# Performance work log

Hardware: AMD Instinct MI355X
Metric: run time of the kernel (lower is better)

Reference implementation:

```python
import jax, jax.numpy as jnp
import numpy as np

B, L, D_MODEL, N_HEADS = 2, 2048, 1024, 16
RANK = max(N_HEADS, int(D_MODEL * 0.25))            # 256
RANK_PER_HEAD = RANK // N_HEADS                      # 16
HEAD_DIM = D_MODEL // N_HEADS                        # 64


def _rope_cos_sin(L, head_dim, dtype=jnp.float32):
    half = head_dim // 2
    theta = 1.0 / (10000.0 ** (jnp.arange(half, dtype=dtype) / half))
    angles = jnp.arange(L, dtype=dtype)[:, None] * theta[None, :]   # [L, half]
    return jnp.cos(angles), jnp.sin(angles)


def _apply_rope(x, cos, sin):
    # x: [B, L, H, D]; pairs (even, odd) rotated by per-position angle.
    B, L, H, D = x.shape
    xp = x.reshape(B, L, H, D // 2, 2)
    x0, x1 = xp[..., 0], xp[..., 1]
    c = cos[None, :, None, :]
    s = sin[None, :, None, :]
    r0 = x0 * c - x1 * s
    r1 = x0 * s + x1 * c
    return jnp.stack([r0, r1], axis=-1).reshape(B, L, H, D)


def setup_inputs() -> dict:
    key = jax.random.key(0)
    ks = jax.random.split(key, 7)
    x = jax.random.normal(ks[0], (B, L, D_MODEL), dtype=jnp.float32)
    mask = jax.random.randint(ks[1], (B, L), 0, 2, dtype=jnp.int32)
    scale = 0.02
    Wq = jax.random.normal(ks[2], (RANK, D_MODEL), dtype=jnp.float32) * scale
    Wk = jax.random.normal(ks[3], (RANK, D_MODEL), dtype=jnp.float32) * scale
    Wv = jax.random.normal(ks[4], (RANK, D_MODEL), dtype=jnp.float32) * scale
    xav_u = float(np.sqrt(6.0 / (HEAD_DIM + RANK_PER_HEAD)))
    U = jax.random.uniform(ks[5], (N_HEADS, HEAD_DIM, RANK_PER_HEAD), dtype=jnp.float32, minval=-xav_u, maxval=xav_u)
    V = jax.random.uniform(ks[6], (N_HEADS, RANK_PER_HEAD, HEAD_DIM), dtype=jnp.float32, minval=-xav_u, maxval=xav_u)
    return {"x": x, "Wq": Wq, "Wk": Wk, "Wv": Wv, "U": U, "V": V, "mask": mask}


def reference(x, Wq, Wk, Wv, U, V, mask):
    Bq, Lq, _ = x.shape
    H, HD, RH = U.shape
    q_low = (x @ Wq.T).reshape(Bq, Lq, H, RH)
    k_low = (x @ Wk.T).reshape(Bq, Lq, H, RH)
    v_low = (x @ Wv.T).reshape(Bq, Lq, H, RH)
    # up-project q/k to head_dim via shared U
    q = jnp.einsum('hdr,blhr->blhd', U, q_low)
    k = jnp.einsum('hdr,blhr->blhd', U, k_low)
    cos, sin = _rope_cos_sin(Lq, HD, x.dtype)
    q = _apply_rope(q, cos, sin)
    k = _apply_rope(k, cos, sin)
    attn = jnp.einsum('blhd,bmhd->bhlm', q, k) / jnp.sqrt(jnp.asarray(HD, x.dtype))
    key_mask = mask.astype(bool)[:, None, None, :]           # [B,1,1,M]
    attn = jnp.where(key_mask, attn, jnp.asarray(-jnp.inf, attn.dtype))
    attn = jax.nn.softmax(attn, axis=-1)
    out = jnp.einsum('bhlm,bmhr->blhr', attn, v_low)
    out = jnp.einsum('blhr,hrd->blhd', out, V)
    return out.reshape(Bq, Lq, H * HD)
```

## Files before the change

kernel.cpp:

```cpp
#include <hip/hip_runtime.h>
#include <hip/hip_bf16.h>

typedef unsigned short u16;
typedef unsigned int u32;
typedef __bf16 bf16x8 __attribute__((ext_vector_type(8)));
typedef float f32x4 __attribute__((ext_vector_type(4)));

#define NB 2
#define NL 2048
#define NDM 1024
#define NH 16
#define NHD 64
#define NRH 16
#define NCOL 2304

#define QSCL 0.18033688011112042f

#define AS1(p) ((const __attribute__((address_space(1))) void*)(p))
#define AS3(p) ((__attribute__((address_space(3))) void*)(p))

__device__ __forceinline__ u16 f2bf(float f) {
  u32 u = __builtin_bit_cast(u32, f);
  u32 r = (u + 0x7fffu + ((u >> 16) & 1u)) >> 16;
  return (u16)r;
}
__device__ __forceinline__ float bf2f(u16 b) {
  return __builtin_bit_cast(float, (u32)b << 16);
}

__global__ void k_prep_weff(const float* __restrict__ Wq, const float* __restrict__ Wk,
                            const float* __restrict__ Wv, const float* __restrict__ U,
                            u16* __restrict__ Wall) {
  int idx = blockIdx.x * 256 + threadIdx.x;
  int col = idx & 1023;
  int row = idx >> 10;
  float acc;
  if (row < 2048) {
    const float* W = (row < 1024) ? Wq : Wk;
    int rr = row & 1023;
    int h = rr >> 6, d = rr & 63;
    const float* Uh = U + (h * NHD + d) * NRH;
    const float* Wr = W + (size_t)(h * NRH) * NDM + col;
    acc = 0.f;
#pragma unroll
    for (int r = 0; r < 16; ++r) acc += Uh[r] * Wr[(size_t)r * NDM];
  } else {
    acc = Wv[(size_t)(row - 2048) * NDM + col];
  }
  Wall[idx] = f2bf(acc);
}

__global__ void k_cast_x(const float* __restrict__ x, u16* __restrict__ xb) {
  int i = blockIdx.x * 256 + threadIdx.x;
  float2 v = *(const float2*)(x + (size_t)i * 2);
  ushort2 o;
  o.x = f2bf(v.x);
  o.y = f2bf(v.y);
  *(ushort2*)(xb + (size_t)i * 2) = o;
}

__global__ void k_rope_tab(float* __restrict__ ctab, float* __restrict__ stab) {
  int i = blockIdx.x * 256 + threadIdx.x;
  if (i >= NL * 32) return;
  int l = i >> 5, j = i & 31;
  float theta = 1.0f / powf(10000.0f, (float)j * (1.0f / 32.0f));
  float ang = (float)l * theta;
  ctab[i] = cosf(ang);
  stab[i] = sinf(ang);
}

__global__ void k_fbias(const int* __restrict__ mask, float* __restrict__ fb) {
  int i = blockIdx.x * 256 + threadIdx.x;
  fb[i] = mask[i] ? 0.f : -1e30f;
}

__global__ __launch_bounds__(256) void k_gemm(const u16* __restrict__ A,
                                              const u16* __restrict__ Bm,
                                              u16* __restrict__ C) {
  __shared__ char lds[32768];
  const int tid = threadIdx.x;
  const int wave = tid >> 6, lane = tid & 63;
  const int bm = blockIdx.x, bn = blockIdx.y;
  const int wr = wave >> 1, wc = wave & 1;
  const char* Ag = (const char*)(A + (size_t)bm * 128 * NDM);
  const char* Bg = (const char*)(Bm + (size_t)bn * 128 * NDM);
  f32x4 acc[4][4] = {};
  for (int kt = 0; kt < 16; ++kt) {
    __syncthreads();
#pragma unroll
    for (int i = 0; i < 4; ++i) {
      int off = wave * 4096 + i * 1024 + lane * 16;
      int src = off ^ ((off >> 3) & 0x70);
      int ga = (src >> 7) * 2048 + kt * 128 + (src & 127);
      __builtin_amdgcn_global_load_lds(AS1(Ag + ga), AS3(lds + wave * 4096 + i * 1024), 16, 0, 0);
      __builtin_amdgcn_global_load_lds(AS1(Bg + ga), AS3(lds + 16384 + wave * 4096 + i * 1024), 16, 0, 0);
    }
    __syncthreads();
#pragma unroll
    for (int kk = 0; kk < 2; ++kk) {
      bf16x8 af[4], bfr[4];
#pragma unroll
      for (int m = 0; m < 4; ++m) {
        int row = wr * 64 + m * 16 + (lane & 15);
        int byte = row * 128 + kk * 64 + ((lane >> 4) << 4);
        af[m] = *(const bf16x8*)(lds + (byte ^ ((row & 7) << 4)));
      }
#pragma unroll
      for (int n = 0; n < 4; ++n) {
        int row = wc * 64 + n * 16 + (lane & 15);
        int byte = row * 128 + kk * 64 + ((lane >> 4) << 4);
        bfr[n] = *(const bf16x8*)(lds + 16384 + (byte ^ ((row & 7) << 4)));
      }
#pragma unroll
      for (int m = 0; m < 4; ++m)
#pragma unroll
        for (int n = 0; n < 4; ++n)
          acc[m][n] = __builtin_amdgcn_mfma_f32_16x16x32_bf16(af[m], bfr[n], acc[m][n], 0, 0, 0);
    }
  }
  const int r0 = bm * 128 + wr * 64, c0 = bn * 128 + wc * 64;
#pragma unroll
  for (int m = 0; m < 4; ++m)
#pragma unroll
    for (int n = 0; n < 4; ++n)
#pragma unroll
      for (int r = 0; r < 4; ++r) {
        int row = r0 + m * 16 + ((lane >> 4) << 2) + r;
        int col = c0 + n * 16 + (lane & 15);
        C[(size_t)row * NCOL + col] = f2bf(acc[m][n][r]);
      }
}

__global__ void k_rope(const u16* __restrict__ pre, const float* __restrict__ ctab,
                       const float* __restrict__ stab, u16* __restrict__ qt,
                       u16* __restrict__ kt) {
  int i = blockIdx.x * 256 + threadIdx.x;
  int j = i & 31, hh = (i >> 5) & 15, l = (i >> 9) & 2047, b = i >> 20;
  float c = ctab[l * 32 + j], s = stab[l * 32 + j];
  const u16* prow = pre + (size_t)(b * NL + l) * NCOL;
  size_t oidx = ((size_t)((b * NH + hh) * NL + l)) * 64 + 2 * j;
  u16 a0 = prow[hh * 64 + 2 * j], a1 = prow[hh * 64 + 2 * j + 1];
  float x0 = bf2f(a0), x1 = bf2f(a1);
  qt[oidx] = f2bf((x0 * c - x1 * s) * QSCL);
  qt[oidx + 1] = f2bf((x0 * s + x1 * c) * QSCL);
  u16 b0 = prow[1024 + hh * 64 + 2 * j], b1 = prow[1024 + hh * 64 + 2 * j + 1];
  x0 = bf2f(b0);
  x1 = bf2f(b1);
  kt[oidx] = f2bf(x0 * c - x1 * s);
  kt[oidx + 1] = f2bf(x0 * s + x1 * c);
}

__global__ void k_vt(const u16* __restrict__ pre, u16* __restrict__ vT) {
  int i = blockIdx.x * 256 + threadIdx.x;
  int l = i & 2047, r = (i >> 11) & 15, h = (i >> 15) & 15, b = i >> 19;
  vT[i] = pre[(size_t)(b * NL + l) * NCOL + 2048 + h * NRH + r];
}

__global__ __launch_bounds__(256) void k_attn(const u16* __restrict__ qt,
                                              const u16* __restrict__ ktp,
                                              const u16* __restrict__ vT,
                                              const float* __restrict__ fbias,
                                              float* __restrict__ Oattn) {
  __shared__ char lds[28672];
  const int tid = threadIdx.x, wave = tid >> 6, lane = tid & 63;
  int blk = (int)blockIdx.x;
  blk = (blk & 7) * 128 + (blk >> 3);
  const int qtile = blk & 31, h = (blk >> 5) & 15, b = blk >> 9;
  const size_t bh = (size_t)(b * NH + h);
  const u16* Q = qt + (bh * NL + (size_t)qtile * 64) * 64;
  const u16* K = ktp + bh * NL * 64;
  const u16* Vt = vT + bh * NRH * NL;
  const float* fbb = fbias + b * NL;
  char* Pl = lds + 20480 + wave * 2048;

  const int g = lane >> 4, qi = lane & 15;
  const int swq = (qi & 7) << 4;

  const int qr = wave * 16 + qi;
  bf16x8 qf0 = *(const bf16x8*)(Q + qr * 64 + g * 8);
  bf16x8 qf1 = *(const bf16x8*)(Q + qr * 64 + 32 + g * 8);

  f32x4 o = {0.f, 0.f, 0.f, 0.f};
  float M = -1e30f, Ls = 0.f;

  const int vr = tid >> 4, vcb = (tid & 15) * 8;
  const int vdst = vr * 128 + vcb;
  const int vswz = vdst ^ ((vr & 7) << 4);

  {
    uint2 vreg = *(const uint2*)((const char*)(Vt + (size_t)vr * NL) + vcb);
    const char* Kg = (const char*)K;
#pragma unroll
    for (int i = 0; i < 2; ++i) {
      int off = wave * 2048 + i * 1024 + lane * 16;
      int src = off ^ ((off >> 3) & 0x70);
      __builtin_amdgcn_global_load_lds(AS1(Kg + src), AS3(lds + wave * 2048 + i * 1024), 16, 0, 0);
    }
    *(uint2*)(lds + 16384 + vswz) = vreg;
  }

  int cur = 0;
  for (int t = 0; t < 32; ++t) {
    __syncthreads();
    const char* Kcur = lds + cur * 8192;
    const char* Vcur = lds + 16384 + cur * 2048;

    const float* fbp = fbb + t * 64 + g * 4;
    f32x4 fb0 = *(const f32x4*)(fbp);
    f32x4 fb1 = *(const f32x4*)(fbp + 16);
    f32x4 fb2 = *(const f32x4*)(fbp + 32);
    f32x4 fb3 = *(const f32x4*)(fbp + 48);
    uint2 vreg;
    if (t < 31) {
      vreg = *(const uint2*)((const char*)(Vt + (size_t)vr * NL) + (t + 1) * 128 + vcb);
      const char* Kg = (const char*)(K + (size_t)(t + 1) * 64 * 64);
      char* Knxt = lds + (cur ^ 1) * 8192;
#pragma unroll
      for (int i = 0; i < 2; ++i) {
        int off = wave * 2048 + i * 1024 + lane * 16;
        int src = off ^ ((off >> 3) & 0x70);
        __builtin_amdgcn_global_load_lds(AS1(Kg + src), AS3(Knxt + wave * 2048 + i * 1024), 16, 0, 0);
      }
    }

    f32x4 s0, s1, s2, s3;
#define QK(n, dst, fbv)                                                    \
  {                                                                        \
    int row = n * 16 + qi;                                                 \
    int base = row * 128 + 16 * g;                                         \
    bf16x8 k0 = *(const bf16x8*)(Kcur + (base ^ swq));                     \
    bf16x8 k1 = *(const bf16x8*)(Kcur + ((base + 64) ^ swq));              \
    f32x4 z = {0.f, 0.f, 0.f, 0.f};                                        \
    z = __builtin_amdgcn_mfma_f32_16x16x32_bf16(k0, qf0, z, 0, 0, 0);      \
    z = __builtin_amdgcn_mfma_f32_16x16x32_bf16(k1, qf1, z, 0, 0, 0);      \
    dst[0] = z[0] + fbv[0]; dst[1] = z[1] + fbv[1];                        \
    dst[2] = z[2] + fbv[2]; dst[3] = z[3] + fbv[3];                        \
  }
    QK(0, s0, fb0) QK(1, s1, fb1) QK(2, s2, fb2) QK(3, s3, fb3)
#undef QK

    float m0 = fmaxf(fmaxf(s0[0], s0[1]), fmaxf(s0[2], s0[3]));
    float m1 = fmaxf(fmaxf(s1[0], s1[1]), fmaxf(s1[2], s1[3]));
    float m2 = fmaxf(fmaxf(s2[0], s2[1]), fmaxf(s2[2], s2[3]));
    float m3 = fmaxf(fmaxf(s3[0], s3[1]), fmaxf(s3[2], s3[3]));
    float mt = fmaxf(fmaxf(m0, m1), fmaxf(m2, m3));
    mt = fmaxf(mt, __shfl_xor(mt, 16));
    mt = fmaxf(mt, __shfl_xor(mt, 32));
    float Mn = fmaxf(M, mt);
    float e = exp2f(M - Mn);
    M = Mn;

    uint2 w0, w1, w2, w3;
    float rs = 0.f;
#define PP(sv, wv)                                                          \
  {                                                                         \
    float p0 = exp2f(sv[0] - M), p1 = exp2f(sv[1] - M);                     \
    float p2 = exp2f(sv[2] - M), p3 = exp2f(sv[3] - M);                     \
    u32 b0 = f2bf(p0), b1 = f2bf(p1), b2 = f2bf(p2), b3 = f2bf(p3);         \
    wv.x = b0 | (b1 << 16);                                                 \
    wv.y = b2 | (b3 << 16);                                                 \
    rs += __builtin_bit_cast(float, b0 << 16);                              \
    rs += __builtin_bit_cast(float, b1 << 16);                              \
    rs += __builtin_bit_cast(float, b2 << 16);                              \
    rs += __builtin_bit_cast(float, b3 << 16);                              \
  }
    PP(s0, w0) PP(s1, w1) PP(s2, w2) PP(s3, w3)
#undef PP
    rs += __shfl_xor(rs, 16);
    rs += __shfl_xor(rs, 32);
    Ls = Ls * e + rs;

    {
      int d0 = qi * 128 + 8 * g;
      *(uint2*)(Pl + ((d0) ^ swq)) = w0;
      *(uint2*)(Pl + ((d0 + 32) ^ swq)) = w1;
      *(uint2*)(Pl + ((d0 + 64) ^ swq)) = w2;
      *(uint2*)(Pl + ((d0 + 96) ^ swq)) = w3;
    }

    if (t < 31) *(uint2*)(lds + 16384 + (cur ^ 1) * 2048 + vswz) = vreg;

#pragma unroll
    for (int i = 0; i < 4; ++i) {
      float ei = __shfl(e, g * 4 + i);
      o[i] *= ei;
    }

#pragma unroll
    for (int c = 0; c < 2; ++c) {
      int ab = qi * 128 + 16 * g + 64 * c;
      int sa = ab ^ swq;
      bf16x8 pf = *(const bf16x8*)(Pl + sa);
      bf16x8 vf = *(const bf16x8*)(Vcur + sa);
      o = __builtin_amdgcn_mfma_f32_16x16x32_bf16(pf, vf, o, 0, 0, 0);
    }
    cur ^= 1;
  }

  const size_t qrow0 = bh * NL + (size_t)qtile * 64 + wave * 16;
#pragma unroll
  for (int i = 0; i < 4; ++i) {
    float Li = __shfl(Ls, g * 4 + i);
    Oattn[(qrow0 + g * 4 + i) * NRH + qi] = o[i] / Li;
  }
}

__global__ void k_proj(const float* __restrict__ Oattn, const float* __restrict__ V,
                       float* __restrict__ out) {
  int bl = blockIdx.x;
  int b = bl >> 11, l = bl & 2047;
  __shared__ float sO[256];
  int tid = threadIdx.x;
  sO[tid] = Oattn[((size_t)(b * NH + (tid >> 4)) * NL + l) * NRH + (tid & 15)];
  __syncthreads();
#pragma unroll
  for (int p = 0; p < 4; ++p) {
    int h = (tid >> 6) + p * 4;
    int d = tid & 63;
    float acc = 0.f;
    const float* Vh = V + (size_t)(h * NRH) * NHD + d;
    const float* Oh = sO + h * NRH;
#pragma unroll
    for (int r = 0; r < 16; ++r) acc += Oh[r] * Vh[(size_t)r * NHD];
    out[(size_t)bl * NDM + h * NHD + d] = acc;
  }
}

extern "C" void kernel_launch(void* const* d_in, const int* in_sizes, int n_in,
                              void* d_out, int out_size, void* d_ws, size_t ws_size,
                              hipStream_t stream) {
  (void)in_sizes; (void)n_in; (void)out_size; (void)ws_size;
  const float* x  = (const float*)d_in[0];
  const float* Wq = (const float*)d_in[1];
  const float* Wk = (const float*)d_in[2];
  const float* Wv = (const float*)d_in[3];
  const float* U  = (const float*)d_in[4];
  const float* Vm = (const float*)d_in[5];
  const int* mask = (const int*)d_in[6];
  float* out = (float*)d_out;
  char* ws = (char*)d_ws;

  u16* Wall   = (u16*)(ws);
  u16* xb     = (u16*)(ws + 4718592);
  u16* pre    = (u16*)(ws + 13107200);
  u16* qt     = (u16*)(ws + 31981568);
  u16* ktb    = (u16*)(ws + 40370176);
  u16* vT     = (u16*)(ws + 48758784);
  float* ctab = (float*)(ws + 50855936);
  float* stab = (float*)(ws + 51118080);
  float* Oattn = (float*)(ws + 4718592);
  float* fbias = (float*)(ws + 8912896);

  k_prep_weff<<<dim3(9216), dim3(256), 0, stream>>>(Wq, Wk, Wv, U, Wall);
  k_cast_x<<<dim3(8192), dim3(256), 0, stream>>>(x, xb);
  k_rope_tab<<<dim3(256), dim3(256), 0, stream>>>(ctab, stab);
  k_gemm<<<dim3(32, 18), dim3(256), 0, stream>>>(xb, Wall, pre);
  k_fbias<<<dim3(16), dim3(256), 0, stream>>>(mask, fbias);
  k_rope<<<dim3(8192), dim3(256), 0, stream>>>(pre, ctab, stab, qt, ktb);
  k_vt<<<dim3(4096), dim3(256), 0, stream>>>(pre, vT);
  k_attn<<<dim3(1024), dim3(256), 0, stream>>>(qt, ktb, vT, fbias, Oattn);
  k_proj<<<dim3(4096), dim3(256), 0, stream>>>(Oattn, Vm, out);
}
```

Baseline: 153.2 us.

## Keep softmax probabilities in registers and pre-permute V to skip LDS round trip

The attention kernel no longer writes P to LDS and reads it back. The bf16-packed probabilities are used directly as the MFMA A operand. To make that work, k_vt now writes V transposed in a key-permuted order that matches the register layout, staged through a shared-memory tile, and V is loaded straight from global memory instead of being double-buffered in LDS. It also adds a lazy rescale that only updates the running max when it grows by more than 8 in log2 units, and it sums the row total in fp32 before rounding. This shrinks LDS use and removes LDS traffic and a barrier dependency, at the cost of uncoalesced-looking global V loads inside the loop and slightly different numerics.

```diff
diff --git a/kernel.cpp b/kernel.cpp
--- a/kernel.cpp
+++ b/kernel.cpp
@@ -26,6 +26,9 @@
 }
 __device__ __forceinline__ float bf2f(u16 b) {
   return __builtin_bit_cast(float, (u32)b << 16);
+}
+__device__ __forceinline__ u32 pk2(float lo, float hi) {
+  return (u32)f2bf(lo) | ((u32)f2bf(hi) << 16);
 }
 
 __global__ void k_prep_weff(const float* __restrict__ Wq, const float* __restrict__ Wk,
@@ -151,9 +154,26 @@
 }
 
 __global__ void k_vt(const u16* __restrict__ pre, u16* __restrict__ vT) {
-  int i = blockIdx.x * 256 + threadIdx.x;
-  int l = i & 2047, r = (i >> 11) & 15, h = (i >> 15) & 15, b = i >> 19;
-  vT[i] = pre[(size_t)(b * NL + l) * NCOL + 2048 + h * NRH + r];
+  __shared__ u16 s[64][16];
+  int blk = blockIdx.x;
+  int t = blk & 31, h = (blk >> 5) & 15, b = blk >> 9;
+  int tid = threadIdx.x;
+  {
+    int l = tid >> 2, rq = (tid & 3) * 4;
+    const u16* src = pre + (size_t)(b * NL + t * 64 + l) * NCOL + 2048 + h * NRH + rq;
+    *(uint2*)&s[l][rq] = *(const uint2*)src;
+  }
+  __syncthreads();
+  {
+    int r = tid >> 4, pq = (tid & 15) * 4;
+    int kb = ((pq >> 5) & 1) * 16 + ((pq >> 2) & 1) * 32 + ((pq >> 3) & 3) * 4;
+    ushort4 o;
+    o.x = s[kb + 0][r];
+    o.y = s[kb + 1][r];
+    o.z = s[kb + 2][r];
+    o.w = s[kb + 3][r];
+    *(ushort4*)(vT + ((size_t)((b * NH + h) * NRH + r)) * NL + t * 64 + pq) = o;
+  }
 }
 
 __global__ __launch_bounds__(256) void k_attn(const u16* __restrict__ qt,
@@ -161,7 +181,7 @@
                                               const u16* __restrict__ vT,
                                               const float* __restrict__ fbias,
                                               float* __restrict__ Oattn) {
-  __shared__ char lds[28672];
+  __shared__ char lds[16384];
   const int tid = threadIdx.x, wave = tid >> 6, lane = tid & 63;
   int blk = (int)blockIdx.x;
   blk = (blk & 7) * 128 + (blk >> 3);
@@ -171,7 +191,6 @@
   const u16* K = ktp + bh * NL * 64;
   const u16* Vt = vT + bh * NRH * NL;
   const float* fbb = fbias + b * NL;
-  char* Pl = lds + 20480 + wave * 2048;
 
   const int g = lane >> 4, qi = lane & 15;
   const int swq = (qi & 7) << 4;
@@ -183,53 +202,53 @@
   f32x4 o = {0.f, 0.f, 0.f, 0.f};
   float M = -1e30f, Ls = 0.f;
 
-  const int vr = tid >> 4, vcb = (tid & 15) * 8;
-  const int vdst = vr * 128 + vcb;
-  const int vswz = vdst ^ ((vr & 7) << 4);
-
-  {
-    uint2 vreg = *(const uint2*)((const char*)(Vt + (size_t)vr * NL) + vcb);
-    const char* Kg = (const char*)K;
-#pragma unroll
-    for (int i = 0; i < 2; ++i) {
-      int off = wave * 2048 + i * 1024 + lane * 16;
-      int src = off ^ ((off >> 3) & 0x70);
-      __builtin_amdgcn_global_load_lds(AS1(Kg + src), AS3(lds + wave * 2048 + i * 1024), 16, 0, 0);
-    }
-    *(uint2*)(lds + 16384 + vswz) = vreg;
+  const u16* Vrow = Vt + (size_t)qi * NL + g * 8;
+  const float* fbg = fbb + g * 4;
+  int koff[4][2];
+#pragma unroll
+  for (int n = 0; n < 4; ++n)
+#pragma unroll
+    for (int dc = 0; dc < 2; ++dc)
+      koff[n][dc] = (((n * 16 + qi) * 128 + dc * 64 + g * 16) ^ swq);
+
+#pragma unroll
+  for (int i = 0; i < 2; ++i) {
+    int off = wave * 2048 + i * 1024 + lane * 16;
+    int src = off ^ ((off >> 3) & 0x70);
+    __builtin_amdgcn_global_load_lds(AS1((const char*)K + src),
+                                     AS3(lds + wave * 2048 + i * 1024), 16, 0, 0);
   }
 
   int cur = 0;
   for (int t = 0; t < 32; ++t) {
     __syncthreads();
-    const char* Kcur = lds + cur * 8192;
-    const char* Vcur = lds + 16384 + cur * 2048;
-
-    const float* fbp = fbb + t * 64 + g * 4;
-    f32x4 fb0 = *(const f32x4*)(fbp);
-    f32x4 fb1 = *(const f32x4*)(fbp + 16);
-    f32x4 fb2 = *(const f32x4*)(fbp + 32);
-    f32x4 fb3 = *(const f32x4*)(fbp + 48);
-    uint2 vreg;
     if (t < 31) {
-      vreg = *(const uint2*)((const char*)(Vt + (size_t)vr * NL) + (t + 1) * 128 + vcb);
-      const char* Kg = (const char*)(K + (size_t)(t + 1) * 64 * 64);
-      char* Knxt = lds + (cur ^ 1) * 8192;
+      const char* Kg = (const char*)(K + (size_t)(t + 1) * 4096);
+      char* Kn = lds + (cur ^ 1) * 8192;
 #pragma unroll
       for (int i = 0; i < 2; ++i) {
         int off = wave * 2048 + i * 1024 + lane * 16;
         int src = off ^ ((off >> 3) & 0x70);
-        __builtin_amdgcn_global_load_lds(AS1(Kg + src), AS3(Knxt + wave * 2048 + i * 1024), 16, 0, 0);
+        __builtin_amdgcn_global_load_lds(AS1(Kg + src),
+                                         AS3(Kn + wave * 2048 + i * 1024), 16, 0, 0);
       }
     }
+    const char* Kcur = lds + cur * 8192;
+
+    const float* fbt = fbg + t * 64;
+    f32x4 fb0 = *(const f32x4*)(fbt);
+    f32x4 fb1 = *(const f32x4*)(fbt + 16);
+    f32x4 fb2 = *(const f32x4*)(fbt + 32);
+    f32x4 fb3 = *(const f32x4*)(fbt + 48);
+    const u16* Vtt = Vrow + t * 64;
+    bf16x8 vf0 = *(const bf16x8*)(Vtt);
+    bf16x8 vf1 = *(const bf16x8*)(Vtt + 32);
 
     f32x4 s0, s1, s2, s3;
 #define QK(n, dst, fbv)                                                    \
   {                                                                        \
-    int row = n * 16 + qi;                                                 \
-    int base = row * 128 + 16 * g;                                         \
-    bf16x8 k0 = *(const bf16x8*)(Kcur + (base ^ swq));                     \
-    bf16x8 k1 = *(const bf16x8*)(Kcur + ((base + 64) ^ swq));              \
+    bf16x8 k0 = *(const bf16x8*)(Kcur + koff[n][0]);                       \
+    bf16x8 k1 = *(const bf16x8*)(Kcur + koff[n][1]);                       \
     f32x4 z = {0.f, 0.f, 0.f, 0.f};                                        \
     z = __builtin_amdgcn_mfma_f32_16x16x32_bf16(k0, qf0, z, 0, 0, 0);      \
     z = __builtin_amdgcn_mfma_f32_16x16x32_bf16(k1, qf1, z, 0, 0, 0);      \
@@ -246,54 +265,33 @@
     float mt = fmaxf(fmaxf(m0, m1), fmaxf(m2, m3));
     mt = fmaxf(mt, __shfl_xor(mt, 16));
     mt = fmaxf(mt, __shfl_xor(mt, 32));
-    float Mn = fmaxf(M, mt);
-    float e = exp2f(M - Mn);
-    M = Mn;
-
-    uint2 w0, w1, w2, w3;
-    float rs = 0.f;
-#define PP(sv, wv)                                                          \
-  {                                                                         \
-    float p0 = exp2f(sv[0] - M), p1 = exp2f(sv[1] - M);                     \
-    float p2 = exp2f(sv[2] - M), p3 = exp2f(sv[3] - M);                     \
-    u32 b0 = f2bf(p0), b1 = f2bf(p1), b2 = f2bf(p2), b3 = f2bf(p3);         \
-    wv.x = b0 | (b1 << 16);                                                 \
-    wv.y = b2 | (b3 << 16);                                                 \
-    rs += __builtin_bit_cast(float, b0 << 16);                              \
-    rs += __builtin_bit_cast(float, b1 << 16);                              \
-    rs += __builtin_bit_cast(float, b2 << 16);                              \
-    rs += __builtin_bit_cast(float, b3 << 16);                              \
-  }
-    PP(s0, w0) PP(s1, w1) PP(s2, w2) PP(s3, w3)
-#undef PP
+
+    if (__any(mt > M + 8.f)) {
+      float Mn = fmaxf(M, mt);
+      float e = exp2f(M - Mn);
+      M = Mn;
+      Ls *= e;
+#pragma unroll
+      for (int i = 0; i < 4; ++i) o[i] *= __shfl(e, g * 4 + i);
+    }
+
+    float p00 = exp2f(s0[0] - M), p01 = exp2f(s0[1] - M), p02 = exp2f(s0[2] - M), p03 = exp2f(s0[3] - M);
+    float p10 = exp2f(s1[0] - M), p11 = exp2f(s1[1] - M), p12 = exp2f(s1[2] - M), p13 = exp2f(s1[3] - M);
+    float p20 = exp2f(s2[0] - M), p21 = exp2f(s2[1] - M), p22 = exp2f(s2[2] - M), p23 = exp2f(s2[3] - M);
+    float p30 = exp2f(s3[0] - M), p31 = exp2f(s3[1] - M), p32 = exp2f(s3[2] - M), p33 = exp2f(s3[3] - M);
+    float rs = (((p00 + p01) + (p02 + p03)) + ((p10 + p11) + (p12 + p13))) +
+               (((p20 + p21) + (p22 + p23)) + ((p30 + p31) + (p32 + p33)));
     rs += __shfl_xor(rs, 16);
     rs += __shfl_xor(rs, 32);
-    Ls = Ls * e + rs;
-
-    {
-      int d0 = qi * 128 + 8 * g;
-      *(uint2*)(Pl + ((d0) ^ swq)) = w0;
-      *(uint2*)(Pl + ((d0 + 32) ^ swq)) = w1;
-      *(uint2*)(Pl + ((d0 + 64) ^ swq)) = w2;
-      *(uint2*)(Pl + ((d0 + 96) ^ swq)) = w3;
-    }
-
-    if (t < 31) *(uint2*)(lds + 16384 + (cur ^ 1) * 2048 + vswz) = vreg;
-
-#pragma unroll
-    for (int i = 0; i < 4; ++i) {
-      float ei = __shfl(e, g * 4 + i);
-      o[i] *= ei;
-    }
-
-#pragma unroll
-    for (int c = 0; c < 2; ++c) {
-      int ab = qi * 128 + 16 * g + 64 * c;
-      int sa = ab ^ swq;
-      bf16x8 pf = *(const bf16x8*)(Pl + sa);
-      bf16x8 vf = *(const bf16x8*)(Vcur + sa);
-      o = __builtin_amdgcn_mfma_f32_16x16x32_bf16(pf, vf, o, 0, 0, 0);
-    }
+    Ls += rs;
+
+    uint4 wa{pk2(p00, p01), pk2(p02, p03), pk2(p20, p21), pk2(p22, p23)};
+    uint4 wb{pk2(p10, p11), pk2(p12, p13), pk2(p30, p31), pk2(p32, p33)};
+    bf16x8 pf0 = __builtin_bit_cast(bf16x8, wa);
+    bf16x8 pf1 = __builtin_bit_cast(bf16x8, wb);
+
+    o = __builtin_amdgcn_mfma_f32_16x16x32_bf16(pf0, vf0, o, 0, 0, 0);
+    o = __builtin_amdgcn_mfma_f32_16x16x32_bf16(pf1, vf1, o, 0, 0, 0);
     cur ^= 1;
   }
 
@@ -357,7 +355,7 @@
   k_gemm<<<dim3(32, 18), dim3(256), 0, stream>>>(xb, Wall, pre);
   k_fbias<<<dim3(16), dim3(256), 0, stream>>>(mask, fbias);
   k_rope<<<dim3(8192), dim3(256), 0, stream>>>(pre, ctab, stab, qt, ktb);
-  k_vt<<<dim3(4096), dim3(256), 0, stream>>>(pre, vT);
+  k_vt<<<dim3(1024), dim3(256), 0, stream>>>(pre, vT);
   k_attn<<<dim3(1024), dim3(256), 0, stream>>>(qt, ktb, vT, fbias, Oattn);
   k_proj<<<dim3(4096), dim3(256), 0, stream>>>(Oattn, Vm, out);
 }
```

Result: faster. 141.9 us (-7.3%).
